# Performance work log

Measured on AMD Instinct MI355X. Metric: run time of the kernel, lower is better.

## Reference

```python
import jax, jax.numpy as jnp
import numpy as np

V, D, H, P = 30000, 2048, 512, 196  # vocab, encoder_dim, hidden, num pixels


def setup_inputs() -> dict:
    key = jax.random.key(0)
    ks = jax.random.split(key, 16)
    s = 0.02
    inp = {
        'img_features': jax.random.normal(ks[0], (32, P, D), jnp.float32),
        'captions': jax.random.randint(ks[1], (32, 20), 0, V),
        # LSTMCell: gates order i,f,g,o; weights stored [in, 4H]
        'Wih': jax.random.normal(ks[2], (H + D, 4 * H), jnp.float32) * s,
        'Whh': jax.random.normal(ks[3], (H, 4 * H), jnp.float32) * s,
        'bih': jnp.zeros((4 * H,), jnp.float32),
        'bhh': jnp.zeros((4 * H,), jnp.float32),
        'W_init_h': jax.random.normal(ks[4], (D, H), jnp.float32) * s,
        'b_init_h': jnp.zeros((H,), jnp.float32),
        'W_init_c': jax.random.normal(ks[5], (D, H), jnp.float32) * s,
        'b_init_c': jnp.zeros((H,), jnp.float32),
        'W_fbeta': jax.random.normal(ks[6], (H, D), jnp.float32) * s,
        'b_fbeta': jnp.zeros((D,), jnp.float32),
        'W_out': jax.random.normal(ks[7], (H, V), jnp.float32) * s,
        'b_out': jnp.zeros((V,), jnp.float32),
        'W_att_img': jax.random.normal(ks[8], (D, H), jnp.float32) * s,
        'b_att_img': jnp.zeros((H,), jnp.float32),
        'W_att_h': jax.random.normal(ks[9], (H, H), jnp.float32) * s,
        'b_att_h': jnp.zeros((H,), jnp.float32),
        'v_att': jax.random.normal(ks[10], (H, 1), jnp.float32) * s,
        'b_v_att': jnp.zeros((1,), jnp.float32),
        'E': jax.random.normal(ks[11], (V, H), jnp.float32) * s,
    }
    return inp


def reference(img_features, captions, Wih, Whh, bih, bhh, W_init_h, b_init_h,
              W_init_c, b_init_c, W_fbeta, b_fbeta, W_out, b_out,
              W_att_img, b_att_img, W_att_h, b_att_h, v_att, b_v_att, E):
    # init LSTM state from mean pooled image features
    avg = img_features.mean(axis=1)                      # [B,D]
    h0 = jnp.tanh(avg @ W_init_h + b_init_h)             # [B,H]
    c0 = jnp.tanh(avg @ W_init_c + b_init_c)
    att_img = img_features @ W_att_img + b_att_img       # [B,P,H] precomputed
    emb = E[captions]                                    # [B,T,H]
    T = captions.shape[1] - 1                            # max_timespan

    def step(carry, emb_t):
        h, c = carry
        # soft attention
        att = jnp.tanh(att_img + (h @ W_att_h + b_att_h)[:, None, :])  # [B,P,H]
        e = jnp.squeeze(att @ v_att, -1) + b_v_att                     # [B,P]
        alpha = jax.nn.softmax(e, axis=-1)
        context = jnp.einsum('bp,bpd->bd', alpha, img_features)        # [B,D]
        gate = jax.nn.sigmoid(h @ W_fbeta + b_fbeta)                   # [B,D]
        x = jnp.concatenate([emb_t, gate * context], axis=1)           # [B,H+D]
        gates = x @ Wih + h @ Whh + bih + bhh                          # [B,4H]
        i, f, g, o = jnp.split(gates, 4, axis=1)
        c = jax.nn.sigmoid(f) * c + jax.nn.sigmoid(i) * jnp.tanh(g)
        h = jax.nn.sigmoid(o) * jnp.tanh(c)
        out = h @ W_out + b_out                                        # [B,V] (dropout=identity)
        return (h, c), (out, alpha)

    emb_t = jnp.swapaxes(emb[:, :T], 0, 1)               # [T,B,H]
    _, (preds, alphas) = jax.lax.scan(step, (h0, c0), emb_t)
    preds = jnp.swapaxes(preds, 0, 1)                    # [B,T,V]
    alphas = jnp.swapaxes(alphas, 0, 1)                  # [B,T,P]
    return preds, alphas
```

## Files before the change

### kernel.cpp

```cpp
#include <hip/hip_runtime.h>
#include <hip/hip_bf16.h>

#define BB_ 32
#define PP_ 196
#define DD_ 2048
#define HH_ 512
#define VV_ 30000
#define TT_ 19
#define KX_ 2560
#define KG_ 3072
#define NTV_ 1875
#define NBOUT_ 469

typedef __attribute__((ext_vector_type(8))) short bf16x8;
typedef __attribute__((ext_vector_type(4))) float f32x4;

__device__ __forceinline__ unsigned short bf16b(float x) {
    __hip_bfloat16 h = __float2bfloat16(x);
    unsigned short u; __builtin_memcpy(&u, &h, 2); return u;
}
__device__ __forceinline__ float b2f(unsigned short u) {
    unsigned int v = (unsigned int)u << 16;
    return __uint_as_float(v);
}
__device__ __forceinline__ float sigf(float x) { return 1.f / (1.f + __expf(-x)); }
__device__ __forceinline__ float ftanh(float x) {
    return 1.f - 2.f / (__expf(2.f * x) + 1.f);
}


__global__ __launch_bounds__(256) void k_cvt8(const float* __restrict__ src,
                                              unsigned short* __restrict__ dst) {
    size_t i0 = ((size_t)blockIdx.x * 256 + threadIdx.x) * 8;
    float4 a = *(const float4*)&src[i0];
    float4 b = *(const float4*)&src[i0 + 4];
    bf16x8 v;
    v[0]=bf16b(a.x); v[1]=bf16b(a.y); v[2]=bf16b(a.z); v[3]=bf16b(a.w);
    v[4]=bf16b(b.x); v[5]=bf16b(b.y); v[6]=bf16b(b.z); v[7]=bf16b(b.w);
    *(bf16x8*)&dst[i0] = v;
}

__global__ __launch_bounds__(256) void k_cvt_nsplit(const float* __restrict__ A, int NA,
        const float* __restrict__ Bp, int NB, int K, unsigned short* __restrict__ dst) {
    int gid = blockIdx.x * 256 + threadIdx.x;
    int lane = gid & 63, rest = gid >> 6;
    int KS = K >> 5;
    int ks = rest % KS, nt = rest / KS;
    int g = lane >> 4, r = lane & 15;
    int k0 = ks * 32 + g * 8;
    int n = nt * 16 + r;
    const float* src; int stride, col;
    if (n < NA) { src = A; stride = NA; col = n; }
    else        { src = Bp; stride = NB; col = n - NA; }
    bf16x8 v;
#pragma unroll
    for (int i = 0; i < 8; i++)
        v[i] = bf16b(src[(size_t)(k0 + i) * stride + col]);
    *(bf16x8*)&dst[(size_t)gid * 8] = v;
}

__global__ __launch_bounds__(256) void k_cvt_ksplit(const float* __restrict__ A, int KA,
        const float* __restrict__ Bp, int K, int N, unsigned short* __restrict__ dst) {
    int gid = blockIdx.x * 256 + threadIdx.x;
    int lane = gid & 63, rest = gid >> 6;
    int KS = K >> 5;
    int ks = rest % KS, nt = rest / KS;
    int g = lane >> 4, r = lane & 15;
    int k0 = ks * 32 + g * 8;
    int n = nt * 16 + r;
    bf16x8 v;
#pragma unroll
    for (int i = 0; i < 8; i++) {
        int k = k0 + i;
        const float* src = (k < KA) ? &A[(size_t)k * N] : &Bp[(size_t)(k - KA) * N];
        v[i] = bf16b(src[n]);
    }
    *(bf16x8*)&dst[(size_t)gid * 8] = v;
}


__global__ __launch_bounds__(256) void k_meanpool(const unsigned short* __restrict__ imgb,
                                                  float* __restrict__ avg) {
    int idx = blockIdx.x * 256 + threadIdx.x;
    int b = idx >> 11, d = idx & 2047;
    const unsigned short* p = imgb + (size_t)b * PP_ * DD_ + d;
    float s = 0.f;
    for (int i = 0; i < PP_; i++) s += b2f(p[(size_t)i * DD_]);
    avg[idx] = s * (1.0f / PP_);
}

__global__ __launch_bounds__(256) void k_init(const float* __restrict__ avg,
        const float* __restrict__ Wh, const float* __restrict__ bh,
        const float* __restrict__ Wc, const float* __restrict__ bc,
        float* __restrict__ c, unsigned short* __restrict__ hb,
        unsigned short* __restrict__ xhb) {
    int idx = blockIdx.x * 256 + threadIdx.x;
    int which = idx >> 14;
    int r = idx & 16383;
    int b = r >> 9, j = r & 511;
    const float* W = which ? Wc : Wh;
    const float* avgb = avg + b * DD_;
    float acc = which ? bc[j] : bh[j];
    for (int d = 0; d < DD_; d++) acc += avgb[d] * W[(size_t)d * HH_ + j];
    float v = tanhf(acc);
    if (which) c[r] = v;
    else { hb[r] = bf16b(v); xhb[b * KG_ + KX_ + j] = bf16b(v); }
}

__global__ __launch_bounds__(256) void k_attimg_mfma(const unsigned short* __restrict__ imgb,
        const unsigned short* __restrict__ waf, const float* __restrict__ bias,
        float* __restrict__ Cout) {
    int wid = blockIdx.x * 4 + (threadIdx.x >> 6);
    int lane = threadIdx.x & 63;
    int g = lane >> 4, r = lane & 15;
    int mblk = wid >> 4, nblk = wid & 15;
    int m0 = mblk * 32, nt0 = nblk * 2;
    f32x4 acc[2][2] = {};
    const unsigned short* a_base = imgb + (size_t)(m0 + r) * DD_ + g * 8;
#pragma unroll 4
    for (int ks = 0; ks < DD_ / 32; ks++) {
        bf16x8 a0 = *(const bf16x8*)(a_base + ks * 32);
        bf16x8 a1 = *(const bf16x8*)(a_base + 16 * DD_ + ks * 32);
        bf16x8 b0 = *(const bf16x8*)(waf + ((size_t)((nt0 + 0) * 64 + ks) * 64 + lane) * 8);
        bf16x8 b1 = *(const bf16x8*)(waf + ((size_t)((nt0 + 1) * 64 + ks) * 64 + lane) * 8);
        acc[0][0] = __builtin_amdgcn_mfma_f32_16x16x32_bf16(a0, b0, acc[0][0], 0, 0, 0);
        acc[0][1] = __builtin_amdgcn_mfma_f32_16x16x32_bf16(a0, b1, acc[0][1], 0, 0, 0);
        acc[1][0] = __builtin_amdgcn_mfma_f32_16x16x32_bf16(a1, b0, acc[1][0], 0, 0, 0);
        acc[1][1] = __builtin_amdgcn_mfma_f32_16x16x32_bf16(a1, b1, acc[1][1], 0, 0, 0);
    }
#pragma unroll
    for (int mi = 0; mi < 2; mi++)
#pragma unroll
        for (int ni = 0; ni < 2; ni++) {
            int n = (nt0 + ni) * 16 + r;
            float bn = bias[n];
#pragma unroll
            for (int j = 0; j < 4; j++) {
                int m = m0 + 16 * mi + 4 * g + j;
                Cout[(size_t)m * HH_ + n] = acc[mi][ni][j] + bn;
            }
        }
}


__device__ __forceinline__ void hmats_body(int wid, int lane,
        const unsigned short* __restrict__ hb, const unsigned short* __restrict__ whf,
        const float* __restrict__ bah, const float* __restrict__ bfb,
        float* __restrict__ hWatt, float* __restrict__ gate) {
    int g = lane >> 4, r = lane & 15;
    f32x4 acc[2] = {};
    const unsigned short* a_base = hb + (size_t)r * HH_ + g * 8;
#pragma unroll
    for (int ks = 0; ks < HH_ / 32; ks++) {
        bf16x8 a0 = *(const bf16x8*)(a_base + ks * 32);
        bf16x8 a1 = *(const bf16x8*)(a_base + 16 * HH_ + ks * 32);
        bf16x8 bf = *(const bf16x8*)(whf + ((size_t)(wid * 16 + ks) * 64 + lane) * 8);
        acc[0] = __builtin_amdgcn_mfma_f32_16x16x32_bf16(a0, bf, acc[0], 0, 0, 0);
        acc[1] = __builtin_amdgcn_mfma_f32_16x16x32_bf16(a1, bf, acc[1], 0, 0, 0);
    }
    int n = wid * 16 + r;
#pragma unroll
    for (int a = 0; a < 2; a++)
#pragma unroll
        for (int j = 0; j < 4; j++) {
            int m = 16 * a + 4 * g + j;
            float v = acc[a][j];
            if (n < HH_) hWatt[m * HH_ + n] = v + bah[n];
            else gate[m * DD_ + (n - HH_)] = sigf(v + bfb[n - HH_]);
        }
}

__global__ __launch_bounds__(256) void k_hmats_mfma(const unsigned short* __restrict__ hb,
        const unsigned short* __restrict__ whf, const float* __restrict__ bah,
        const float* __restrict__ bfb, float* __restrict__ hWatt, float* __restrict__ gate) {
    int wid = blockIdx.x * 4 + (threadIdx.x >> 6);
    hmats_body(wid, threadIdx.x & 63, hb, whf, bah, bfb, hWatt, gate);
}

__global__ __launch_bounds__(256) void k_energy(const float* __restrict__ att_img,
        const float* __restrict__ hWatt, const float* __restrict__ v_att,
        const float* __restrict__ b_v, float* __restrict__ e) {
    int wave = threadIdx.x >> 6, lane = threadIdx.x & 63;
    int gp = blockIdx.x * 4 + wave;
    int b = gp / PP_;
    const float* ai = att_img + (size_t)gp * HH_;
    const float* hw = hWatt + (size_t)b * HH_;
    float acc = 0.f;
#pragma unroll
    for (int rep = 0; rep < 2; rep++) {
        int j = rep * 256 + lane * 4;
        float4 a4 = *(const float4*)&ai[j];
        float4 h4 = *(const float4*)&hw[j];
        float4 v4 = *(const float4*)&v_att[j];
        acc += v4.x * ftanh(a4.x + h4.x);
        acc += v4.y * ftanh(a4.y + h4.y);
        acc += v4.z * ftanh(a4.z + h4.z);
        acc += v4.w * ftanh(a4.w + h4.w);
    }
    for (int off = 32; off > 0; off >>= 1) acc += __shfl_down(acc, off);
    if (lane == 0) e[gp] = acc + b_v[0];
}

__global__ __launch_bounds__(128) void k_softmax_ctx(const float* __restrict__ e,
        const unsigned short* __restrict__ imgb, const float* __restrict__ gate,
        const float* __restrict__ Emb, const int* __restrict__ captions, int t,
        unsigned short* __restrict__ xhb, const unsigned short* __restrict__ hb,
        float* __restrict__ alpha_out) {
    __shared__ float sa[PP_];
    __shared__ float red[128];
    const int b = blockIdx.x, dc = blockIdx.y, tid = threadIdx.x;
    const float* eb = e + b * PP_;
    float e0 = eb[tid];
    float e1 = (tid < PP_ - 128) ? eb[128 + tid] : -1e30f;
    red[tid] = fmaxf(e0, e1);
    __syncthreads();
    for (int s = 64; s > 0; s >>= 1) {
        if (tid < s) red[tid] = fmaxf(red[tid], red[tid + s]);
        __syncthreads();
    }
    float mx = red[0];
    __syncthreads();
    float p0 = __expf(e0 - mx);
    float p1 = (tid < PP_ - 128) ? __expf(e1 - mx) : 0.f;
    red[tid] = p0 + p1;
    __syncthreads();
    for (int s = 64; s > 0; s >>= 1) {
        if (tid < s) red[tid] += red[tid + s];
        __syncthreads();
    }
    float inv = 1.f / red[0];
    sa[tid] = p0 * inv;
    if (tid < PP_ - 128) sa[128 + tid] = p1 * inv;
    __syncthreads();
    int d0 = dc * 256 + tid * 2;
    const unsigned short* ib = imgb + (size_t)b * PP_ * DD_ + d0;
    float acc0 = 0.f, acc1 = 0.f;
#pragma unroll 4
    for (int p = 0; p < PP_; p++) {
        unsigned int v = *(const unsigned int*)&ib[(size_t)p * DD_];
        float s = sa[p];
        acc0 += s * __uint_as_float(v << 16);
        acc1 += s * __uint_as_float(v & 0xffff0000u);
    }
    float2 gv = *(const float2*)&gate[b * DD_ + d0];
    unsigned int packed = (unsigned int)bf16b(gv.x * acc0)
                        | ((unsigned int)bf16b(gv.y * acc1) << 16);
    *(unsigned int*)&xhb[b * KG_ + HH_ + d0] = packed;
    if (dc == 0) {
        float* ao = alpha_out + ((size_t)b * TT_ + t) * PP_;
        ao[tid] = sa[tid];
        if (tid < PP_ - 128) ao[128 + tid] = sa[128 + tid];
        int tok = captions[b * 20 + t];
        float4 ev = *(const float4*)&Emb[(size_t)tok * HH_ + tid * 4];
        unsigned short* xo = xhb + b * KG_ + tid * 4;
        xo[0] = bf16b(ev.x); xo[1] = bf16b(ev.y);
        xo[2] = bf16b(ev.z); xo[3] = bf16b(ev.w);
    } else if (dc == 1) {
        *(uint2*)&xhb[b * KG_ + KX_ + tid * 4] =
            *(const uint2*)&hb[b * HH_ + tid * 4];
    }
}

__global__ __launch_bounds__(256) void k_gateslstm(const unsigned short* __restrict__ xhb,
        const unsigned short* __restrict__ wgf, const float* __restrict__ bih,
        const float* __restrict__ bhh, float* __restrict__ c,
        unsigned short* __restrict__ hb) {
    __shared__ float lds_g[4][BB_][16];
    int q = threadIdx.x >> 6;
    int lane = threadIdx.x & 63;
    int g = lane >> 4, r = lane & 15;
    int jb = blockIdx.x;
    int nt = q * 32 + jb;
    f32x4 acc[2] = {};
    const unsigned short* a_base = xhb + (size_t)r * KG_ + g * 8;
#pragma unroll 4
    for (int ks = 0; ks < KG_ / 32; ks++) {
        bf16x8 a0 = *(const bf16x8*)(a_base + ks * 32);
        bf16x8 a1 = *(const bf16x8*)(a_base + 16 * KG_ + ks * 32);
        bf16x8 bf = *(const bf16x8*)(wgf + ((size_t)(nt * 96 + ks) * 64 + lane) * 8);
        acc[0] = __builtin_amdgcn_mfma_f32_16x16x32_bf16(a0, bf, acc[0], 0, 0, 0);
        acc[1] = __builtin_amdgcn_mfma_f32_16x16x32_bf16(a1, bf, acc[1], 0, 0, 0);
    }
#pragma unroll
    for (int a = 0; a < 2; a++)
#pragma unroll
        for (int j = 0; j < 4; j++)
            lds_g[q][16 * a + 4 * g + j][r] = acc[a][j];
    __syncthreads();
#pragma unroll
    for (int it = 0; it < 2; it++) {
        int e2 = threadIdx.x + it * 256;
        int m = e2 >> 4, jc = e2 & 15;
        int jg = jb * 16 + jc;
        float gi = lds_g[0][m][jc] + bih[jg] + bhh[jg];
        float gf = lds_g[1][m][jc] + bih[HH_ + jg] + bhh[HH_ + jg];
        float gg = lds_g[2][m][jc] + bih[2 * HH_ + jg] + bhh[2 * HH_ + jg];
        float go = lds_g[3][m][jc] + bih[3 * HH_ + jg] + bhh[3 * HH_ + jg];
        int ci = m * HH_ + jg;
        float cn = sigf(gf) * c[ci] + sigf(gi) * ftanh(gg);
        float hn = sigf(go) * ftanh(cn);
        c[ci] = cn;
        hb[ci] = bf16b(hn);
    }
}

__global__ __launch_bounds__(256) void k_out_hmats(const unsigned short* __restrict__ hb,
        const unsigned short* __restrict__ wof, const float* __restrict__ bout,
        const unsigned short* __restrict__ whf, const float* __restrict__ bah,
        const float* __restrict__ bfb, float* __restrict__ preds,
        float* __restrict__ hWatt, float* __restrict__ gate, int t) {
    int lane = threadIdx.x & 63;
    int wv = threadIdx.x >> 6;
    if (blockIdx.x >= NBOUT_) {
        int wid = (blockIdx.x - NBOUT_) * 4 + wv;
        hmats_body(wid, lane, hb, whf, bah, bfb, hWatt, gate);
        return;
    }
    int nt = blockIdx.x * 4 + wv;
    if (nt >= NTV_) return;
    int g = lane >> 4, r = lane & 15;
    f32x4 acc[2] = {};
    const unsigned short* a_base = hb + (size_t)r * HH_ + g * 8;
#pragma unroll
    for (int ks = 0; ks < HH_ / 32; ks++) {
        bf16x8 a0 = *(const bf16x8*)(a_base + ks * 32);
        bf16x8 a1 = *(const bf16x8*)(a_base + 16 * HH_ + ks * 32);
        bf16x8 bf = *(const bf16x8*)(wof + ((size_t)(nt * 16 + ks) * 64 + lane) * 8);
        acc[0] = __builtin_amdgcn_mfma_f32_16x16x32_bf16(a0, bf, acc[0], 0, 0, 0);
        acc[1] = __builtin_amdgcn_mfma_f32_16x16x32_bf16(a1, bf, acc[1], 0, 0, 0);
    }
    int n = nt * 16 + r;
    float bn = bout[n];
#pragma unroll
    for (int a = 0; a < 2; a++)
#pragma unroll
        for (int j = 0; j < 4; j++) {
            int m = 16 * a + 4 * g + j;
            preds[((size_t)m * TT_ + t) * VV_ + n] = acc[a][j] + bn;
        }
}


extern "C" void kernel_launch(void* const* d_in, const int* in_sizes, int n_in,
                              void* d_out, int out_size, void* d_ws, size_t ws_size,
                              hipStream_t stream) {
    const float* img     = (const float*)d_in[0];
    const int*   caps    = (const int*)d_in[1];
    const float* Wih     = (const float*)d_in[2];
    const float* Whh     = (const float*)d_in[3];
    const float* bih     = (const float*)d_in[4];
    const float* bhh     = (const float*)d_in[5];
    const float* Winh    = (const float*)d_in[6];
    const float* binh    = (const float*)d_in[7];
    const float* Winc    = (const float*)d_in[8];
    const float* binc    = (const float*)d_in[9];
    const float* Wfb     = (const float*)d_in[10];
    const float* bfb     = (const float*)d_in[11];
    const float* Wout    = (const float*)d_in[12];
    const float* bout    = (const float*)d_in[13];
    const float* Wai     = (const float*)d_in[14];
    const float* bai     = (const float*)d_in[15];
    const float* Wah     = (const float*)d_in[16];
    const float* bah     = (const float*)d_in[17];
    const float* v_att   = (const float*)d_in[18];
    const float* b_v     = (const float*)d_in[19];
    const float* Emb     = (const float*)d_in[20];

    float* preds  = (float*)d_out;
    float* alphas = (float*)d_out + (size_t)BB_ * TT_ * VV_;

    char* w = (char*)d_ws;
    size_t off = 0;
    auto alloc = [&](size_t bytes) {
        char* p = w + off;
        off += (bytes + 255) & ~(size_t)255;
        return p;
    };
    unsigned short* imgb = (unsigned short*)alloc((size_t)BB_ * PP_ * DD_ * 2);
    unsigned short* wof  = (unsigned short*)alloc((size_t)HH_ * VV_ * 2);
    unsigned short* wgf  = (unsigned short*)alloc((size_t)KG_ * 2048 * 2);
    unsigned short* waf  = (unsigned short*)alloc((size_t)DD_ * HH_ * 2);
    unsigned short* whf  = (unsigned short*)alloc((size_t)HH_ * KX_ * 2);
    float* att_img = (float*)alloc((size_t)BB_ * PP_ * HH_ * 4);
    float* avg     = (float*)alloc((size_t)BB_ * DD_ * 4);
    float* c       = (float*)alloc((size_t)BB_ * HH_ * 4);
    float* hWatt   = (float*)alloc((size_t)BB_ * HH_ * 4);
    float* gate    = (float*)alloc((size_t)BB_ * DD_ * 4);
    float* e       = (float*)alloc((size_t)BB_ * PP_ * 4);
    unsigned short* hb  = (unsigned short*)alloc((size_t)BB_ * HH_ * 2);
    unsigned short* xhb = (unsigned short*)alloc((size_t)BB_ * KG_ * 2);
    (void)ws_size;

    k_cvt8<<<6272, 256, 0, stream>>>(img, imgb);
    k_cvt_nsplit<<<7500, 256, 0, stream>>>(Wout, VV_, Wout, 0, HH_, wof);
    k_cvt_nsplit<<<512, 256, 0, stream>>>(Wai, HH_, Wai, 0, DD_, waf);
    k_cvt_nsplit<<<640, 256, 0, stream>>>(Wah, HH_, Wfb, DD_, HH_, whf);
    k_cvt_ksplit<<<3072, 256, 0, stream>>>(Wih, KX_, Whh, KG_, 2048, wgf);
    k_meanpool<<<256, 256, 0, stream>>>(imgb, avg);
    k_init<<<128, 256, 0, stream>>>(avg, Winh, binh, Winc, binc, c, hb, xhb);
    k_attimg_mfma<<<784, 256, 0, stream>>>(imgb, waf, bai, att_img);
    k_hmats_mfma<<<40, 256, 0, stream>>>(hb, whf, bah, bfb, hWatt, gate);

    for (int t = 0; t < TT_; t++) {
        k_energy<<<1568, 256, 0, stream>>>(att_img, hWatt, v_att, b_v, e);
        k_softmax_ctx<<<dim3(BB_, 8), 128, 0, stream>>>(e, imgb, gate, Emb, caps, t,
                                                        xhb, hb, alphas);
        k_gateslstm<<<32, 256, 0, stream>>>(xhb, wgf, bih, bhh, c, hb);
        k_out_hmats<<<509, 256, 0, stream>>>(hb, wof, bout, whf, bah, bfb,
                                             preds, hWatt, gate, t);
    }
}
```

Baseline: 1.813 ms.

## Fuse setup conversions, energy+softmax+context per step, split-K LSTM gates

Merges all weight/image bf16 conversion launches into one kernel and replaces the scalar init GEMV with an MFMA kernel fed by a bf16 mean pool computed directly from fp32 input. Stores att_img in bf16 and fuses the energy, softmax and context computation into one per-step kernel, which removes a launch and the e buffer round-trip but uses only 64 blocks. The LSTM gate kernel now uses 1024 threads with a 4-way K split reduced through LDS. This trades grid parallelism and some precision for fewer launches and less memory traffic.

Result: slower. 2.228 ms (+22.9%).

```diff
diff --git a/kernel.cpp b/kernel.cpp
--- a/kernel.cpp
+++ b/kernel.cpp
@@ -20,8 +20,7 @@
     unsigned short u; __builtin_memcpy(&u, &h, 2); return u;
 }
 __device__ __forceinline__ float b2f(unsigned short u) {
-    unsigned int v = (unsigned int)u << 16;
-    return __uint_as_float(v);
+    return __uint_as_float((unsigned int)u << 16);
 }
 __device__ __forceinline__ float sigf(float x) { return 1.f / (1.f + __expf(-x)); }
 __device__ __forceinline__ float ftanh(float x) {
@@ -29,9 +28,9 @@
 }
 
 
-__global__ __launch_bounds__(256) void k_cvt8(const float* __restrict__ src,
-                                              unsigned short* __restrict__ dst) {
-    size_t i0 = ((size_t)blockIdx.x * 256 + threadIdx.x) * 8;
+__device__ __forceinline__ void d_cvt8(int bid, int tid,
+        const float* __restrict__ src, unsigned short* __restrict__ dst) {
+    size_t i0 = ((size_t)bid * 256 + tid) * 8;
     float4 a = *(const float4*)&src[i0];
     float4 b = *(const float4*)&src[i0 + 4];
     bf16x8 v;
@@ -40,9 +39,10 @@
     *(bf16x8*)&dst[i0] = v;
 }
 
-__global__ __launch_bounds__(256) void k_cvt_nsplit(const float* __restrict__ A, int NA,
-        const float* __restrict__ Bp, int NB, int K, unsigned short* __restrict__ dst) {
-    int gid = blockIdx.x * 256 + threadIdx.x;
+__device__ __forceinline__ void d_nsplit(int bid, int tid,
+        const float* __restrict__ A, int NA, const float* __restrict__ Bp, int NB,
+        int K, unsigned short* __restrict__ dst) {
+    int gid = bid * 256 + tid;
     int lane = gid & 63, rest = gid >> 6;
     int KS = K >> 5;
     int ks = rest % KS, nt = rest / KS;
@@ -59,9 +59,10 @@
     *(bf16x8*)&dst[(size_t)gid * 8] = v;
 }
 
-__global__ __launch_bounds__(256) void k_cvt_ksplit(const float* __restrict__ A, int KA,
-        const float* __restrict__ Bp, int K, int N, unsigned short* __restrict__ dst) {
-    int gid = blockIdx.x * 256 + threadIdx.x;
+__device__ __forceinline__ void d_ksplit(int bid, int tid,
+        const float* __restrict__ A, int KA, const float* __restrict__ Bp,
+        int K, int N, unsigned short* __restrict__ dst) {
+    int gid = bid * 256 + tid;
     int lane = gid & 63, rest = gid >> 6;
     int KS = K >> 5;
     int ks = rest % KS, nt = rest / KS;
@@ -78,38 +79,76 @@
     *(bf16x8*)&dst[(size_t)gid * 8] = v;
 }
 
-
-__global__ __launch_bounds__(256) void k_meanpool(const unsigned short* __restrict__ imgb,
-                                                  float* __restrict__ avg) {
-    int idx = blockIdx.x * 256 + threadIdx.x;
-    int b = idx >> 11, d = idx & 2047;
-    const unsigned short* p = imgb + (size_t)b * PP_ * DD_ + d;
-    float s = 0.f;
-    for (int i = 0; i < PP_; i++) s += b2f(p[(size_t)i * DD_]);
-    avg[idx] = s * (1.0f / PP_);
-}
-
-__global__ __launch_bounds__(256) void k_init(const float* __restrict__ avg,
-        const float* __restrict__ Wh, const float* __restrict__ bh,
-        const float* __restrict__ Wc, const float* __restrict__ bc,
-        float* __restrict__ c, unsigned short* __restrict__ hb,
-        unsigned short* __restrict__ xhb) {
-    int idx = blockIdx.x * 256 + threadIdx.x;
-    int which = idx >> 14;
-    int r = idx & 16383;
-    int b = r >> 9, j = r & 511;
-    const float* W = which ? Wc : Wh;
-    const float* avgb = avg + b * DD_;
-    float acc = which ? bc[j] : bh[j];
-    for (int d = 0; d < DD_; d++) acc += avgb[d] * W[(size_t)d * HH_ + j];
-    float v = tanhf(acc);
-    if (which) c[r] = v;
-    else { hb[r] = bf16b(v); xhb[b * KG_ + KX_ + j] = bf16b(v); }
+__global__ __launch_bounds__(256) void k_cvt_all(
+        const float* __restrict__ img, unsigned short* __restrict__ imgb,
+        const float* __restrict__ Wout, unsigned short* __restrict__ wof,
+        const float* __restrict__ Wai, unsigned short* __restrict__ waf,
+        const float* __restrict__ Wah, const float* __restrict__ Wfb,
+        unsigned short* __restrict__ whf,
+        const float* __restrict__ Wih, const float* __restrict__ Whh,
+        unsigned short* __restrict__ wgf,
+        const float* __restrict__ Winh, const float* __restrict__ Winc,
+        unsigned short* __restrict__ wif) {
+    int b = blockIdx.x, t = threadIdx.x;
+    if (b < 6272)       d_cvt8(b, t, img, imgb);
+    else if (b < 13772) d_nsplit(b - 6272, t, Wout, VV_, Wout, 0, HH_, wof);
+    else if (b < 14284) d_nsplit(b - 13772, t, Wai, HH_, Wai, 0, DD_, waf);
+    else if (b < 14924) d_nsplit(b - 14284, t, Wah, HH_, Wfb, DD_, HH_, whf);
+    else if (b < 17996) d_ksplit(b - 14924, t, Wih, KX_, Whh, KG_, 2048, wgf);
+    else                d_nsplit(b - 17996, t, Winh, HH_, Winc, HH_, DD_, wif);
+}
+
+
+__global__ __launch_bounds__(256) void k_meanpool(const float* __restrict__ img,
+                                                  unsigned short* __restrict__ avgb) {
+    int b = blockIdx.x, tid = threadIdx.x;
+    int d0 = tid * 8;
+    const float* p = img + (size_t)b * PP_ * DD_ + d0;
+    float s[8] = {};
+    for (int i = 0; i < PP_; i++) {
+        float4 a = *(const float4*)&p[(size_t)i * DD_];
+        float4 c = *(const float4*)&p[(size_t)i * DD_ + 4];
+        s[0]+=a.x; s[1]+=a.y; s[2]+=a.z; s[3]+=a.w;
+        s[4]+=c.x; s[5]+=c.y; s[6]+=c.z; s[7]+=c.w;
+    }
+    bf16x8 v;
+#pragma unroll
+    for (int i = 0; i < 8; i++) v[i] = bf16b(s[i] * (1.0f / PP_));
+    *(bf16x8*)&avgb[b * DD_ + d0] = v;
+}
+
+__global__ __launch_bounds__(256) void k_init_mfma(const unsigned short* __restrict__ avgb,
+        const unsigned short* __restrict__ wif, const float* __restrict__ binh,
+        const float* __restrict__ binc, float* __restrict__ c,
+        unsigned short* __restrict__ hb) {
+    int wid = blockIdx.x * 4 + (threadIdx.x >> 6);
+    int lane = threadIdx.x & 63;
+    int g = lane >> 4, r = lane & 15;
+    f32x4 acc[2] = {};
+    const unsigned short* a_base = avgb + (size_t)r * DD_ + g * 8;
+#pragma unroll 4
+    for (int ks = 0; ks < DD_ / 32; ks++) {
+        bf16x8 a0 = *(const bf16x8*)(a_base + ks * 32);
+        bf16x8 a1 = *(const bf16x8*)(a_base + 16 * DD_ + ks * 32);
+        bf16x8 bf = *(const bf16x8*)(wif + ((size_t)(wid * 64 + ks) * 64 + lane) * 8);
+        acc[0] = __builtin_amdgcn_mfma_f32_16x16x32_bf16(a0, bf, acc[0], 0, 0, 0);
+        acc[1] = __builtin_amdgcn_mfma_f32_16x16x32_bf16(a1, bf, acc[1], 0, 0, 0);
+    }
+    int n = wid * 16 + r;
+#pragma unroll
+    for (int a = 0; a < 2; a++)
+#pragma unroll
+        for (int j = 0; j < 4; j++) {
+            int m = 16 * a + 4 * g + j;
+            float v = ftanh(acc[a][j] + ((n < HH_) ? binh[n] : binc[n - HH_]));
+            if (n < HH_) hb[m * HH_ + n] = bf16b(v);
+            else c[m * HH_ + (n - HH_)] = v;
+        }
 }
 
 __global__ __launch_bounds__(256) void k_attimg_mfma(const unsigned short* __restrict__ imgb,
         const unsigned short* __restrict__ waf, const float* __restrict__ bias,
-        float* __restrict__ Cout) {
+        unsigned short* __restrict__ attb) {
     int wid = blockIdx.x * 4 + (threadIdx.x >> 6);
     int lane = threadIdx.x & 63;
     int g = lane >> 4, r = lane & 15;
@@ -137,7 +176,7 @@
 #pragma unroll
             for (int j = 0; j < 4; j++) {
                 int m = m0 + 16 * mi + 4 * g + j;
-                Cout[(size_t)m * HH_ + n] = acc[mi][ni][j] + bn;
+                attb[(size_t)m * HH_ + n] = bf16b(acc[mi][ni][j] + bn);
             }
         }
 }
@@ -177,104 +216,110 @@
     hmats_body(wid, threadIdx.x & 63, hb, whf, bah, bfb, hWatt, gate);
 }
 
-__global__ __launch_bounds__(256) void k_energy(const float* __restrict__ att_img,
-        const float* __restrict__ hWatt, const float* __restrict__ v_att,
-        const float* __restrict__ b_v, float* __restrict__ e) {
-    int wave = threadIdx.x >> 6, lane = threadIdx.x & 63;
-    int gp = blockIdx.x * 4 + wave;
-    int b = gp / PP_;
-    const float* ai = att_img + (size_t)gp * HH_;
-    const float* hw = hWatt + (size_t)b * HH_;
-    float acc = 0.f;
-#pragma unroll
-    for (int rep = 0; rep < 2; rep++) {
-        int j = rep * 256 + lane * 4;
-        float4 a4 = *(const float4*)&ai[j];
-        float4 h4 = *(const float4*)&hw[j];
-        float4 v4 = *(const float4*)&v_att[j];
-        acc += v4.x * ftanh(a4.x + h4.x);
-        acc += v4.y * ftanh(a4.y + h4.y);
-        acc += v4.z * ftanh(a4.z + h4.z);
-        acc += v4.w * ftanh(a4.w + h4.w);
-    }
-    for (int off = 32; off > 0; off >>= 1) acc += __shfl_down(acc, off);
-    if (lane == 0) e[gp] = acc + b_v[0];
-}
-
-__global__ __launch_bounds__(128) void k_softmax_ctx(const float* __restrict__ e,
-        const unsigned short* __restrict__ imgb, const float* __restrict__ gate,
-        const float* __restrict__ Emb, const int* __restrict__ captions, int t,
-        unsigned short* __restrict__ xhb, const unsigned short* __restrict__ hb,
-        float* __restrict__ alpha_out) {
+__global__ __launch_bounds__(256) void k_step1(const unsigned short* __restrict__ attb,
+        const unsigned short* __restrict__ imgb, const float* __restrict__ hWatt,
+        const float* __restrict__ gate, const float* __restrict__ Emb,
+        const int* __restrict__ captions, const float* __restrict__ v_att,
+        const float* __restrict__ b_v, int t, unsigned short* __restrict__ xhb,
+        const unsigned short* __restrict__ hb, float* __restrict__ alpha_out) {
+    __shared__ float e_lds[PP_];
     __shared__ float sa[PP_];
-    __shared__ float red[128];
+    __shared__ float red[256];
     const int b = blockIdx.x, dc = blockIdx.y, tid = threadIdx.x;
-    const float* eb = e + b * PP_;
-    float e0 = eb[tid];
-    float e1 = (tid < PP_ - 128) ? eb[128 + tid] : -1e30f;
-    red[tid] = fmaxf(e0, e1);
-    __syncthreads();
-    for (int s = 64; s > 0; s >>= 1) {
+    const int wv = tid >> 6, lane = tid & 63;
+    const float* hw = hWatt + (size_t)b * HH_ + lane * 8;
+    float hw8[8], vv8[8];
+    {
+        float4 h0 = *(const float4*)&hw[0];
+        float4 h1 = *(const float4*)&hw[4];
+        const float* vp = v_att + lane * 8;
+        float4 v0 = *(const float4*)&vp[0];
+        float4 v1 = *(const float4*)&vp[4];
+        hw8[0]=h0.x; hw8[1]=h0.y; hw8[2]=h0.z; hw8[3]=h0.w;
+        hw8[4]=h1.x; hw8[5]=h1.y; hw8[6]=h1.z; hw8[7]=h1.w;
+        vv8[0]=v0.x; vv8[1]=v0.y; vv8[2]=v0.z; vv8[3]=v0.w;
+        vv8[4]=v1.x; vv8[5]=v1.y; vv8[6]=v1.z; vv8[7]=v1.w;
+    }
+    float bv0 = b_v[0];
+    const unsigned short* ab = attb + (size_t)b * PP_ * HH_ + lane * 8;
+    for (int i = 0; i < 49; i++) {
+        int p = wv * 49 + i;
+        bf16x8 av = *(const bf16x8*)(ab + (size_t)p * HH_);
+        float acc = 0.f;
+#pragma unroll
+        for (int j = 0; j < 8; j++)
+            acc += vv8[j] * ftanh(b2f((unsigned short)av[j]) + hw8[j]);
+        for (int off = 32; off > 0; off >>= 1) acc += __shfl_down(acc, off);
+        if (lane == 0) e_lds[p] = acc + bv0;
+    }
+    __syncthreads();
+    float ev = (tid < PP_) ? e_lds[tid] : -1e30f;
+    red[tid] = ev;
+    __syncthreads();
+    for (int s = 128; s > 0; s >>= 1) {
         if (tid < s) red[tid] = fmaxf(red[tid], red[tid + s]);
         __syncthreads();
     }
     float mx = red[0];
     __syncthreads();
-    float p0 = __expf(e0 - mx);
-    float p1 = (tid < PP_ - 128) ? __expf(e1 - mx) : 0.f;
-    red[tid] = p0 + p1;
-    __syncthreads();
-    for (int s = 64; s > 0; s >>= 1) {
+    float pv = (tid < PP_) ? __expf(ev - mx) : 0.f;
+    red[tid] = pv;
+    __syncthreads();
+    for (int s = 128; s > 0; s >>= 1) {
         if (tid < s) red[tid] += red[tid + s];
         __syncthreads();
     }
     float inv = 1.f / red[0];
-    sa[tid] = p0 * inv;
-    if (tid < PP_ - 128) sa[128 + tid] = p1 * inv;
-    __syncthreads();
-    int d0 = dc * 256 + tid * 2;
+    if (tid < PP_) sa[tid] = pv * inv;
+    __syncthreads();
+    int d0 = dc * 1024 + tid * 4;
     const unsigned short* ib = imgb + (size_t)b * PP_ * DD_ + d0;
-    float acc0 = 0.f, acc1 = 0.f;
+    float a0 = 0.f, a1 = 0.f, a2 = 0.f, a3 = 0.f;
 #pragma unroll 4
     for (int p = 0; p < PP_; p++) {
-        unsigned int v = *(const unsigned int*)&ib[(size_t)p * DD_];
+        uint2 v = *(const uint2*)&ib[(size_t)p * DD_];
         float s = sa[p];
-        acc0 += s * __uint_as_float(v << 16);
-        acc1 += s * __uint_as_float(v & 0xffff0000u);
-    }
-    float2 gv = *(const float2*)&gate[b * DD_ + d0];
-    unsigned int packed = (unsigned int)bf16b(gv.x * acc0)
-                        | ((unsigned int)bf16b(gv.y * acc1) << 16);
-    *(unsigned int*)&xhb[b * KG_ + HH_ + d0] = packed;
+        a0 += s * __uint_as_float(v.x << 16);
+        a1 += s * __uint_as_float(v.x & 0xffff0000u);
+        a2 += s * __uint_as_float(v.y << 16);
+        a3 += s * __uint_as_float(v.y & 0xffff0000u);
+    }
+    float4 gv = *(const float4*)&gate[b * DD_ + d0];
+    unsigned int u01 = (unsigned int)bf16b(gv.x * a0) | ((unsigned int)bf16b(gv.y * a1) << 16);
+    unsigned int u23 = (unsigned int)bf16b(gv.z * a2) | ((unsigned int)bf16b(gv.w * a3) << 16);
+    *(uint2*)&xhb[b * KG_ + HH_ + d0] = make_uint2(u01, u23);
     if (dc == 0) {
-        float* ao = alpha_out + ((size_t)b * TT_ + t) * PP_;
-        ao[tid] = sa[tid];
-        if (tid < PP_ - 128) ao[128 + tid] = sa[128 + tid];
-        int tok = captions[b * 20 + t];
-        float4 ev = *(const float4*)&Emb[(size_t)tok * HH_ + tid * 4];
-        unsigned short* xo = xhb + b * KG_ + tid * 4;
-        xo[0] = bf16b(ev.x); xo[1] = bf16b(ev.y);
-        xo[2] = bf16b(ev.z); xo[3] = bf16b(ev.w);
-    } else if (dc == 1) {
-        *(uint2*)&xhb[b * KG_ + KX_ + tid * 4] =
-            *(const uint2*)&hb[b * HH_ + tid * 4];
-    }
-}
-
-__global__ __launch_bounds__(256) void k_gateslstm(const unsigned short* __restrict__ xhb,
+        if (tid < PP_) alpha_out[((size_t)b * TT_ + t) * PP_ + tid] = sa[tid];
+        if (tid < 128) {
+            int tok = captions[b * 20 + t];
+            float4 evec = *(const float4*)&Emb[(size_t)tok * HH_ + tid * 4];
+            unsigned int e01 = (unsigned int)bf16b(evec.x) | ((unsigned int)bf16b(evec.y) << 16);
+            unsigned int e23 = (unsigned int)bf16b(evec.z) | ((unsigned int)bf16b(evec.w) << 16);
+            *(uint2*)&xhb[b * KG_ + tid * 4] = make_uint2(e01, e23);
+        } else {
+            int i = tid - 128;
+            *(uint2*)&xhb[b * KG_ + KX_ + i * 4] = *(const uint2*)&hb[b * HH_ + i * 4];
+        }
+    }
+}
+
+__global__ __launch_bounds__(1024) void k_gateslstm(const unsigned short* __restrict__ xhb,
         const unsigned short* __restrict__ wgf, const float* __restrict__ bih,
         const float* __restrict__ bhh, float* __restrict__ c,
         unsigned short* __restrict__ hb) {
-    __shared__ float lds_g[4][BB_][16];
-    int q = threadIdx.x >> 6;
-    int lane = threadIdx.x & 63;
-    int g = lane >> 4, r = lane & 15;
-    int jb = blockIdx.x;
-    int nt = q * 32 + jb;
+    __shared__ float part[16][BB_][16];
+    __shared__ float gsum[4][BB_][16];
+    const int tid = threadIdx.x;
+    const int w = tid >> 6, lane = tid & 63;
+    const int q = w & 3, kc = w >> 2;
+    const int g = lane >> 4, r = lane & 15;
+    const int jb = blockIdx.x;
+    const int nt = q * 32 + jb;
     f32x4 acc[2] = {};
     const unsigned short* a_base = xhb + (size_t)r * KG_ + g * 8;
 #pragma unroll 4
-    for (int ks = 0; ks < KG_ / 32; ks++) {
+    for (int i = 0; i < 24; i++) {
+        int ks = kc * 24 + i;
         bf16x8 a0 = *(const bf16x8*)(a_base + ks * 32);
         bf16x8 a1 = *(const bf16x8*)(a_base + 16 * KG_ + ks * 32);
         bf16x8 bf = *(const bf16x8*)(wgf + ((size_t)(nt * 96 + ks) * 64 + lane) * 8);
@@ -285,17 +330,26 @@
     for (int a = 0; a < 2; a++)
 #pragma unroll
         for (int j = 0; j < 4; j++)
-            lds_g[q][16 * a + 4 * g + j][r] = acc[a][j];
-    __syncthreads();
-#pragma unroll
-    for (int it = 0; it < 2; it++) {
-        int e2 = threadIdx.x + it * 256;
-        int m = e2 >> 4, jc = e2 & 15;
+            part[w][16 * a + 4 * g + j][r] = acc[a][j];
+    __syncthreads();
+    {
+        int qq = tid >> 8, s2 = tid & 255;
+        int m = s2 >> 3, j0 = (s2 & 7) * 2;
+#pragma unroll
+        for (int jj = 0; jj < 2; jj++) {
+            int jc = j0 + jj;
+            gsum[qq][m][jc] = part[qq][m][jc] + part[4 + qq][m][jc]
+                            + part[8 + qq][m][jc] + part[12 + qq][m][jc];
+        }
+    }
+    __syncthreads();
+    if (tid < 512) {
+        int m = tid >> 4, jc = tid & 15;
         int jg = jb * 16 + jc;
-        float gi = lds_g[0][m][jc] + bih[jg] + bhh[jg];
-        float gf = lds_g[1][m][jc] + bih[HH_ + jg] + bhh[HH_ + jg];
-        float gg = lds_g[2][m][jc] + bih[2 * HH_ + jg] + bhh[2 * HH_ + jg];
-        float go = lds_g[3][m][jc] + bih[3 * HH_ + jg] + bhh[3 * HH_ + jg];
+        float gi = gsum[0][m][jc] + bih[jg] + bhh[jg];
+        float gf = gsum[1][m][jc] + bih[HH_ + jg] + bhh[HH_ + jg];
+        float gg = gsum[2][m][jc] + bih[2 * HH_ + jg] + bhh[2 * HH_ + jg];
+        float go = gsum[3][m][jc] + bih[3 * HH_ + jg] + bhh[3 * HH_ + jg];
         int ci = m * HH_ + jg;
         float cn = sigf(gf) * c[ci] + sigf(gi) * ftanh(gg);
         float hn = sigf(go) * ftanh(cn);
@@ -381,31 +435,28 @@
     unsigned short* wgf  = (unsigned short*)alloc((size_t)KG_ * 2048 * 2);
     unsigned short* waf  = (unsigned short*)alloc((size_t)DD_ * HH_ * 2);
     unsigned short* whf  = (unsigned short*)alloc((size_t)HH_ * KX_ * 2);
-    float* att_img = (float*)alloc((size_t)BB_ * PP_ * HH_ * 4);
-    float* avg     = (float*)alloc((size_t)BB_ * DD_ * 4);
+    unsigned short* wif  = (unsigned short*)alloc((size_t)DD_ * 1024 * 2);
+    unsigned short* attb = (unsigned short*)alloc((size_t)BB_ * PP_ * HH_ * 2);
+    unsigned short* avgb = (unsigned short*)alloc((size_t)BB_ * DD_ * 2);
     float* c       = (float*)alloc((size_t)BB_ * HH_ * 4);
     float* hWatt   = (float*)alloc((size_t)BB_ * HH_ * 4);
     float* gate    = (float*)alloc((size_t)BB_ * DD_ * 4);
-    float* e       = (float*)alloc((size_t)BB_ * PP_ * 4);
     unsigned short* hb  = (unsigned short*)alloc((size_t)BB_ * HH_ * 2);
     unsigned short* xhb = (unsigned short*)alloc((size_t)BB_ * KG_ * 2);
     (void)ws_size;
 
-    k_cvt8<<<6272, 256, 0, stream>>>(img, imgb);
-    k_cvt_nsplit<<<7500, 256, 0, stream>>>(Wout, VV_, Wout, 0, HH_, wof);
-    k_cvt_nsplit<<<512, 256, 0, stream>>>(Wai, HH_, Wai, 0, DD_, waf);
-    k_cvt_nsplit<<<640, 256, 0, stream>>>(Wah, HH_, Wfb, DD_, HH_, whf);
-    k_cvt_ksplit<<<3072, 256, 0, stream>>>(Wih, KX_, Whh, KG_, 2048, wgf);
-    k_meanpool<<<256, 256, 0, stream>>>(imgb, avg);
-    k_init<<<128, 256, 0, stream>>>(avg, Winh, binh, Winc, binc, c, hb, xhb);
-    k_attimg_mfma<<<784, 256, 0, stream>>>(imgb, waf, bai, att_img);
+    k_cvt_all<<<19020, 256, 0, stream>>>(img, imgb, Wout, wof, Wai, waf,
+                                         Wah, Wfb, whf, Wih, Whh, wgf,
+                                         Winh, Winc, wif);
+    k_meanpool<<<BB_, 256, 0, stream>>>(img, avgb);
+    k_init_mfma<<<16, 256, 0, stream>>>(avgb, wif, binh, binc, c, hb);
+    k_attimg_mfma<<<784, 256, 0, stream>>>(imgb, waf, bai, attb);
     k_hmats_mfma<<<40, 256, 0, stream>>>(hb, whf, bah, bfb, hWatt, gate);
 
     for (int t = 0; t < TT_; t++) {
-        k_energy<<<1568, 256, 0, stream>>>(att_img, hWatt, v_att, b_v, e);
-        k_softmax_ctx<<<dim3(BB_, 8), 128, 0, stream>>>(e, imgb, gate, Emb, caps, t,
-                                                        xhb, hb, alphas);
-        k_gateslstm<<<32, 256, 0, stream>>>(xhb, wgf, bih, bhh, c, hb);
+        k_step1<<<dim3(BB_, 2), 256, 0, stream>>>(attb, imgb, hWatt, gate, Emb,
+                                                  caps, v_att, b_v, t, xhb, hb, alphas);
+        k_gateslstm<<<BB_, 1024, 0, stream>>>(xhb, wgf, bih, bhh, c, hb);
         k_out_hmats<<<509, 256, 0, stream>>>(hb, wof, bout, whf, bah, bfb,
                                              preds, hWatt, gate, t);
     }
```
